# Kernel optimization log

Measured on AMD Instinct MI355X. Metric: run time of the kernel, lower is better.

## Reference

```python
import math
import jax, jax.numpy as jnp
import numpy as np

B, IB, S, D = 8, 1024, 4096, 512
WINDOW = 1
SPARSITY = 2


def setup_inputs() -> dict:
    key = jax.random.key(0)
    ks = jax.random.split(key, 12)
    std = 1.0 / math.sqrt(D)
    std_b2s = 1.0 / math.sqrt(IB)
    return {
        "text_feature": jax.random.normal(ks[0], (B, S, D), jnp.float32),
        "image_feature": jax.random.normal(ks[1], (B, IB, D), jnp.float32),
        "Wq": jax.random.normal(ks[2], (D, D), jnp.float32) * std,
        "bq": jax.random.normal(ks[3], (D,), jnp.float32) * std,
        "Wk": jax.random.normal(ks[4], (D, D), jnp.float32) * std,
        "bk": jax.random.normal(ks[5], (D,), jnp.float32) * std,
        "Wv": jax.random.normal(ks[6], (D, D), jnp.float32) * std,
        "bv": jax.random.normal(ks[7], (D,), jnp.float32) * std,
        # torch Linear(in=IB, out=S): weight shape (S, IB)
        "Wb2s": jax.random.normal(ks[8], (S, IB), jnp.float32) * std_b2s,
        "bb2s": jax.random.normal(ks[9], (S,), jnp.float32) * std_b2s,
    }


def _banded_softmax_weights():
    # attention_mask[i, max(0,i-w):min(S,i+w+1)] = 1 ; since IB < S this is a
    # banded 0/1 matrix over (IB, IB), then row-softmax.
    i = jnp.arange(IB)[:, None]
    j = jnp.arange(IB)[None, :]
    mask = ((j >= i - WINDOW) & (j <= i + WINDOW)).astype(jnp.float32)
    return jax.nn.softmax(mask, axis=-1)  # (IB, IB)


def reference(text_feature, image_feature, Wq, bq, Wk, bk, Wv, bv, Wb2s, bb2s):
    d_k = text_feature.shape[-1]
    q = image_feature @ Wq.T + bq            # (B, IB, D)
    k = text_feature @ Wk.T + bk              # (B, S, D)
    v = text_feature @ Wv.T + bv              # (B, S, D)

    # batch-invariant sparse attention pattern: compute once, broadcast via einsum
    aw = _banded_softmax_weights()             # (IB, IB)
    aw = aw @ Wb2s.T + bb2s                    # (IB, S)
    num_nonzero = S // SPARSITY + 2 * WINDOW
    topk_scores, topk_idx = jax.lax.top_k(aw, num_nonzero)  # (IB, nnz)
    sparse = jnp.zeros((IB, S), aw.dtype).at[jnp.arange(IB)[:, None], topk_idx].set(topk_scores)

    out = jnp.einsum('is,bsd->bid', sparse, k)                       # (B, IB, D)
    out = jnp.einsum('bid,bjd->bij', q, out) / math.sqrt(d_k)        # (B, IB, IB)
    out = out @ Wb2s.T + bb2s                                        # (B, IB, S)
    out = jnp.einsum('bis,bsd->bid', jax.nn.softmax(out, axis=-1), v)  # (B, IB, D)
    return out
```

## Files before the change

### kernel.cpp

```cpp
#include <hip/hip_runtime.h>

#define B_  8
#define IB_ 1024
#define S_  4096
#define D_  512

typedef _Float16 f16;
typedef _Float16 f16x8 __attribute__((ext_vector_type(8)));
typedef _Float16 f16x4 __attribute__((ext_vector_type(4)));
typedef float    f32x4 __attribute__((ext_vector_type(4)));

__device__ __forceinline__ void gld_lds16(const f16* g, f16* l) {
  __builtin_amdgcn_global_load_lds(
      (const __attribute__((address_space(1))) void*)g,
      (__attribute__((address_space(3))) void*)l, 16, 0, 0);
}

__global__ __launch_bounds__(256) void gemm_bt(
    const f16* __restrict__ A, const f16* __restrict__ B,
    float* __restrict__ C32, f16* __restrict__ C16,
    int M, int N, int K, int lda, int ldb, int ksplit,
    long long sAb, long long sBb, long long sCb,
    const float* __restrict__ bias_row, const float* __restrict__ bias_col,
    float scale)
{
  __shared__ f16 ldsA[2][128 * 32];
  __shared__ f16 ldsB[2][128 * 32];
  const int tid  = threadIdx.x;
  const int lane = tid & 63;
  const int wave = tid >> 6;
  const int zb   = blockIdx.z / ksplit;
  const int ks   = blockIdx.z % ksplit;
  A += (size_t)zb * (size_t)sAb;
  B += (size_t)zb * (size_t)sBb;
  const int m0 = blockIdx.y * 128;
  const int n0 = blockIdx.x * 128;
  const int wm = wave >> 1, wn = wave & 1;

  f32x4 acc[4][4];
#pragma unroll
  for (int i = 0; i < 4; ++i)
#pragma unroll
    for (int j = 0; j < 4; ++j) acc[i][j] = (f32x4){0.f, 0.f, 0.f, 0.f};

  int aoff[4], boff[4];
  const int cl = lane >> 4;
#pragma unroll
  for (int r = 0; r < 4; ++r) {
    int rowa = wm * 64 + r * 16 + (lane & 15);
    aoff[r] = rowa * 32 + (cl ^ ((rowa >> 1) & 3)) * 8;
    int rowb = wn * 64 + r * 16 + (lane & 15);
    boff[r] = rowb * 32 + (cl ^ ((rowb >> 1) & 3)) * 8;
  }
  int srow[2], scg[2];
#pragma unroll
  for (int it = 0; it < 2; ++it) {
    int ch = wave * 64 + it * 256 + lane;
    srow[it] = ch >> 2;
    scg[it]  = (ch & 3) ^ ((srow[it] >> 1) & 3);
  }

#define STAGE(bf_, k0_)                                                        \
  do {                                                                         \
    _Pragma("unroll")                                                          \
    for (int it = 0; it < 2; ++it) {                                           \
      gld_lds16(A + (size_t)(m0 + srow[it]) * (size_t)lda +                    \
                    ((k0_) + scg[it] * 8),                                     \
                &ldsA[bf_][(wave * 64 + it * 256) * 8]);                       \
      gld_lds16(B + (size_t)(n0 + srow[it]) * (size_t)ldb +                    \
                    ((k0_) + scg[it] * 8),                                     \
                &ldsB[bf_][(wave * 64 + it * 256) * 8]);                       \
    }                                                                          \
  } while (0)

  const int Kc   = K / ksplit;
  const int kbeg = ks * Kc;
  const int nt   = Kc / 32;

  STAGE(0, kbeg);
  for (int t = 0; t < nt; ++t) {
    const int cur = t & 1;
    if (t + 1 < nt) {
      STAGE(cur ^ 1, kbeg + (t + 1) * 32);
      asm volatile("s_waitcnt vmcnt(4)" ::: "memory");
    } else {
      asm volatile("s_waitcnt vmcnt(0)" ::: "memory");
    }
    __builtin_amdgcn_s_barrier();
    __builtin_amdgcn_sched_barrier(0);
    f16x8 af[4], bf[4];
#pragma unroll
    for (int r = 0; r < 4; ++r) af[r] = *(const f16x8*)&ldsA[cur][aoff[r]];
#pragma unroll
    for (int r = 0; r < 4; ++r) bf[r] = *(const f16x8*)&ldsB[cur][boff[r]];
#pragma unroll
    for (int mr = 0; mr < 4; ++mr)
#pragma unroll
      for (int nr = 0; nr < 4; ++nr)
        acc[mr][nr] = __builtin_amdgcn_mfma_f32_16x16x32_f16(
            af[mr], bf[nr], acc[mr][nr], 0, 0, 0);
    __builtin_amdgcn_sched_barrier(0);
    __builtin_amdgcn_s_barrier();
    __builtin_amdgcn_sched_barrier(0);
  }
#undef STAGE

  const size_t cz = (ksplit > 1) ? (size_t)blockIdx.z : (size_t)zb;
  float* c32 = C32 ? C32 + cz * (size_t)sCb : nullptr;
  f16*   c16 = C16 ? C16 + cz * (size_t)sCb : nullptr;
#pragma unroll
  for (int mr = 0; mr < 4; ++mr) {
#pragma unroll
    for (int r = 0; r < 4; ++r) {
      int grow = m0 + wm * 64 + mr * 16 + (lane >> 4) * 4 + r;
      float brv = bias_row ? bias_row[grow] : 0.f;
#pragma unroll
      for (int nr = 0; nr < 4; ++nr) {
        int gcol = n0 + wn * 64 + nr * 16 + (lane & 15);
        float v = acc[mr][nr][r] * scale + brv +
                  (bias_col ? bias_col[gcol] : 0.f);
        if (c32) c32[(size_t)grow * N + gcol] = v;
        else     c16[(size_t)grow * N + gcol] = (f16)v;
      }
    }
  }
}

__global__ __launch_bounds__(256) void gemm_pt(
    const f16* __restrict__ Bt, const float* __restrict__ uarr,
    const float* __restrict__ inv2, const float* __restrict__ Acs,
    const float* __restrict__ bb2s, f16* __restrict__ parts)
{
  __shared__ f16 ldsA[64 * 32];
  __shared__ f16 ldsB[2][256 * 32];
  __shared__ float cA2[1024], cB2[1024];
  const int tid  = threadIdx.x;
  const int lane = tid & 63;
  const int wave = tid >> 6;
  int id = (int)blockIdx.x;
  id = (id & 7) * 128 + (id >> 3);
  const int zb = id >> 7;
  const int rem = id & 127;
  const int mt = rem >> 3;
  const int x  = (rem >> 2) & 1;
  const int ks = rem & 3;
  const int kbeg = ks * 1024;
  const int m0 = mt * 64, n0 = x * 256;
  const f16* B = Bt + (size_t)zb * ((size_t)D_ * S_);

  const float L2E = 1.44269504088896340736f;
  for (int i = tid; i < 1024; i += 256) {
    cA2[i] = Acs[kbeg + i] * L2E;
    cB2[i] = bb2s[kbeg + i] * L2E;
  }
  const int srowA = tid >> 2;
  const int scgA  = tid & 3;
  const int spcA  = scgA ^ ((srowA >> 1) & 3);
  const float u_  = uarr[zb * IB_ + m0 + srowA];
  const float iv_ = inv2[zb * IB_ + m0 + srowA];
  const int cl = lane >> 4;
  int aoff[4], boff[4];
#pragma unroll
  for (int r = 0; r < 4; ++r) {
    int rowa = r * 16 + (lane & 15);
    aoff[r] = rowa * 32 + (cl ^ ((rowa >> 1) & 3)) * 8;
    int rowb = wave * 64 + r * 16 + (lane & 15);
    boff[r] = rowb * 32 + (cl ^ ((rowb >> 1) & 3)) * 8;
  }
  int srow[4], scg[4];
#pragma unroll
  for (int it = 0; it < 4; ++it) {
    int ch = wave * 64 + it * 256 + lane;
    srow[it] = ch >> 2;
    scg[it]  = (ch & 3) ^ ((srow[it] >> 1) & 3);
  }
  f32x4 acc[4][4];
#pragma unroll
  for (int i = 0; i < 4; ++i)
#pragma unroll
    for (int j = 0; j < 4; ++j) acc[i][j] = (f32x4){0.f, 0.f, 0.f, 0.f};

#define STAGEB(bf_, k0_)                                                       \
  do {                                                                         \
    _Pragma("unroll")                                                          \
    for (int it = 0; it < 4; ++it) {                                           \
      gld_lds16(B + (size_t)(n0 + srow[it]) * (size_t)S_ +                     \
                    ((k0_) + scg[it] * 8),                                     \
                &ldsB[bf_][(wave * 64 + it * 256) * 8]);                       \
    }                                                                          \
  } while (0)

  __syncthreads();
  STAGEB(0, kbeg);
  for (int t = 0; t < 32; ++t) {
    const int cur = t & 1;
    if (t + 1 < 32) STAGEB(cur ^ 1, kbeg + (t + 1) * 32);
    {
      const int kl = t * 32 + scgA * 8;
      f16x8 hp;
#pragma unroll
      for (int j = 0; j < 8; ++j) {
        float e = exp2f(fmaf(u_, cA2[kl + j], cB2[kl + j])) * iv_;
        hp[j] = (f16)e;
      }
      *(f16x8*)&ldsA[srowA * 32 + spcA * 8] = hp;
    }
    asm volatile("s_waitcnt lgkmcnt(0)" ::: "memory");
    __builtin_amdgcn_sched_barrier(0);
    if (t + 1 < 32) asm volatile("s_waitcnt vmcnt(4)" ::: "memory");
    else            asm volatile("s_waitcnt vmcnt(0)" ::: "memory");
    __builtin_amdgcn_s_barrier();
    __builtin_amdgcn_sched_barrier(0);
    f16x8 af[4], bf[4];
#pragma unroll
    for (int r = 0; r < 4; ++r) af[r] = *(const f16x8*)&ldsA[aoff[r]];
#pragma unroll
    for (int r = 0; r < 4; ++r) bf[r] = *(const f16x8*)&ldsB[cur][boff[r]];
    asm volatile("s_waitcnt lgkmcnt(0)" ::: "memory");
    __builtin_amdgcn_sched_barrier(0);
#pragma unroll
    for (int mr = 0; mr < 4; ++mr)
#pragma unroll
      for (int nr = 0; nr < 4; ++nr)
        acc[mr][nr] = __builtin_amdgcn_mfma_f32_16x16x32_f16(
            af[mr], bf[nr], acc[mr][nr], 0, 0, 0);
    __builtin_amdgcn_sched_barrier(0);
    __builtin_amdgcn_s_barrier();
    __builtin_amdgcn_sched_barrier(0);
  }
#undef STAGEB

  f16* cp = parts + (size_t)(zb * 4 + ks) * (size_t)(IB_ * D_);
#pragma unroll
  for (int mr = 0; mr < 4; ++mr) {
#pragma unroll
    for (int rr = 0; rr < 4; ++rr) {
      int grow = m0 + mr * 16 + (lane >> 4) * 4 + rr;
#pragma unroll
      for (int nr = 0; nr < 4; ++nr) {
        int gcol = n0 + wave * 64 + nr * 16 + (lane & 15);
        cp[(size_t)grow * D_ + gcol] = (f16)acc[mr][nr][rr];
      }
    }
  }
}

__global__ __launch_bounds__(256) void reduce_ks4_f16(
    const f16x8* __restrict__ p, f16x8* __restrict__ o, unsigned n8)
{
  const unsigned pb8 = (IB_ * D_) / 8;
  unsigned i = blockIdx.x * 256u + threadIdx.x;
  const unsigned stride = gridDim.x * 256u;
  for (; i < n8; i += stride) {
    unsigned g = i / pb8, r = i - g * pb8;
    size_t base = ((size_t)g * 4u) * pb8 + r;
    float acc[8] = {0.f, 0.f, 0.f, 0.f, 0.f, 0.f, 0.f, 0.f};
#pragma unroll
    for (int ks = 0; ks < 4; ++ks) {
      f16x8 v = p[base + (size_t)ks * pb8];
#pragma unroll
      for (int j = 0; j < 8; ++j) acc[j] += (float)v[j];
    }
    f16x8 h;
#pragma unroll
    for (int j = 0; j < 8; ++j) h[j] = (f16)acc[j];
    o[i] = h;
  }
}

__global__ __launch_bounds__(256) void reduce_ks2_bias(
    const f16x8* __restrict__ p, const float* __restrict__ bias,
    float4* __restrict__ o, unsigned n8)
{
  unsigned i = blockIdx.x * 256u + threadIdx.x;
  const unsigned stride = gridDim.x * 256u;
  for (; i < n8; i += stride) {
    f16x8 a = p[i];
    f16x8 b = p[i + (size_t)n8];
    const int c0 = (int)((i * 8u) & (D_ - 1));
    float4 lo, hi;
    lo.x = (float)a[0] + (float)b[0] + bias[c0 + 0];
    lo.y = (float)a[1] + (float)b[1] + bias[c0 + 1];
    lo.z = (float)a[2] + (float)b[2] + bias[c0 + 2];
    lo.w = (float)a[3] + (float)b[3] + bias[c0 + 3];
    hi.x = (float)a[4] + (float)b[4] + bias[c0 + 4];
    hi.y = (float)a[5] + (float)b[5] + bias[c0 + 5];
    hi.z = (float)a[6] + (float)b[6] + bias[c0 + 6];
    hi.w = (float)a[7] + (float)b[7] + bias[c0 + 7];
    o[(size_t)i * 2]     = lo;
    o[(size_t)i * 2 + 1] = hi;
  }
}

__global__ __launch_bounds__(256) void cvt_f32_to_f16(
    const float* __restrict__ in, f16* __restrict__ out, unsigned n)
{
  unsigned i = (blockIdx.x * 256u + threadIdx.x) * 4u;
  if (i >= n) return;
  const float4 v = *(const float4*)(in + i);
  f16x4 h;
  h[0] = (f16)v.x; h[1] = (f16)v.y; h[2] = (f16)v.z; h[3] = (f16)v.w;
  *(f16x4*)(out + i) = h;
}

__global__ __launch_bounds__(256) void transpose_text(
    const float* __restrict__ in, f16* __restrict__ out)
{
  __shared__ float t[32][65];
  const int b = blockIdx.z;
  const int s0 = blockIdx.x * 64, d0 = blockIdx.y * 32;
  const int dx = threadIdx.x & 31;
  const int sy = threadIdx.x >> 5;
  const float* ip = in + ((size_t)b * S_ + s0) * D_ + d0;
#pragma unroll
  for (int j = 0; j < 8; ++j) {
    int sl = j * 8 + sy;
    t[dx][sl] = ip[(size_t)sl * D_ + dx];
  }
  __syncthreads();
  const int sx = threadIdx.x & 63;
  const int dy = threadIdx.x >> 6;
  f16* op = out + ((size_t)b * D_ + d0) * S_ + s0;
#pragma unroll
  for (int j = 0; j < 8; ++j) {
    int dl = j * 4 + dy;
    op[(size_t)dl * S_ + sx] = (f16)t[dl][sx];
  }
}

__global__ __launch_bounds__(256) void rowsum_kernel(
    const float* __restrict__ W, float* __restrict__ out)
{
  int s = blockIdx.x;
  const float* row = W + (size_t)s * IB_;
  float acc = 0.f;
  for (int j = threadIdx.x; j < IB_; j += 256) acc += row[j];
  __shared__ float red[4];
#pragma unroll
  for (int o = 32; o >= 1; o >>= 1) acc += __shfl_xor(acc, o);
  if ((threadIdx.x & 63) == 0) red[threadIdx.x >> 6] = acc;
  __syncthreads();
  if (threadIdx.x == 0) out[s] = red[0] + red[1] + red[2] + red[3];
}

__device__ __forceinline__ unsigned fkey(float x) {
  unsigned u = __float_as_uint(x);
  return (u & 0x80000000u) ? ~u : (u | 0x80000000u);
}

__global__ __launch_bounds__(256) void prep_mu(
    const float* __restrict__ Acs, const float* __restrict__ bb2s,
    float* __restrict__ muk, float* __restrict__ rhat)
{
  __shared__ float vals[S_];
  __shared__ unsigned hist[256];
  __shared__ unsigned sprefix;
  __shared__ int srem;
  __shared__ float rred[4];
  const float e1 = 2.71828182845904523536f;
  const float Z = 3.f * e1 + (float)(IB_ - 3);
  const float alpha = 1.f / Z;
  for (int s = threadIdx.x; s < S_; s += 256)
    vals[s] = alpha * Acs[s] + bb2s[s];
  if (threadIdx.x == 0) { sprefix = 0u; srem = S_ / 2 + 2; }
  __syncthreads();
  for (int shift = 24; shift >= 0; shift -= 8) {
    hist[threadIdx.x] = 0u;
    __syncthreads();
    unsigned pfx = sprefix;
    unsigned himask = (shift == 24) ? 0u : (0xFFFFFFFFu << (shift + 8));
    for (int s = threadIdx.x; s < S_; s += 256) {
      unsigned key = fkey(vals[s]);
      if ((key & himask) == (pfx & himask))
        atomicAdd(&hist[(key >> shift) & 255u], 1u);
    }
    __syncthreads();
    if (threadIdx.x == 0) {
      int rem = srem;
      unsigned acc = 0;
      int b = 255;
      for (; b > 0; --b) {
        unsigned c = hist[b];
        if (acc + c >= (unsigned)rem) break;
        acc += c;
      }
      sprefix = pfx | ((unsigned)b << shift);
      srem = rem - (int)acc;
    }
    __syncthreads();
  }
  const unsigned T = sprefix;
  float myrs = 0.f;
  for (int s = threadIdx.x; s < S_; s += 256) {
    float v = vals[s];
    bool keep = fkey(v) >= T;
    muk[s] = keep ? v : 0.f;
    if (keep) myrs += v;
  }
#pragma unroll
  for (int o = 32; o >= 1; o >>= 1) myrs += __shfl_xor(myrs, o);
  if ((threadIdx.x & 63) == 0) rred[threadIdx.x >> 6] = myrs;
  __syncthreads();
  if (threadIdx.x == 0) rhat[0] = rred[0] + rred[1] + rred[2] + rred[3];
}

__global__ __launch_bounds__(256) void that_partial(
    const float* __restrict__ text, const float* __restrict__ muk,
    float* __restrict__ tp)
{
  const int d = blockIdx.x * 256 + threadIdx.x;
  const int c = blockIdx.y;
  const int b = blockIdx.z;
  const float* tb = text + ((size_t)b * S_ + (size_t)c * 128) * D_ + d;
  float acc = 0.f;
  for (int s = 0; s < 128; ++s) {
    float m = muk[c * 128 + s];
    if (m != 0.f) acc += m * tb[(size_t)s * D_];
  }
  tp[((size_t)b * 32 + c) * D_ + d] = acc;
}

__global__ __launch_bounds__(256) void tt_reduce(
    const float* __restrict__ tp, float* __restrict__ tt)
{
  const int d = blockIdx.x * 256 + threadIdx.x;
  const int b = blockIdx.y;
  float acc = 0.f;
#pragma unroll
  for (int c = 0; c < 32; ++c) acc += tp[((size_t)b * 32 + c) * D_ + d];
  tt[(size_t)b * D_ + d] = acc;
}

__global__ __launch_bounds__(256) void mhat2_kernel(
    const float* __restrict__ tt, const float* __restrict__ Wk,
    const float* __restrict__ bk, const float* __restrict__ rhat,
    float* __restrict__ mh)
{
  __shared__ float tl[B_ * D_];
  const int t = threadIdx.x;
  for (int i = t; i < B_ * D_; i += 256) tl[i] = tt[i];
  __syncthreads();
  const int r = blockIdx.x;
  const int lane = t & 63, wave = t >> 6;
  const float* wr = Wk + (size_t)r * D_;
  float w[8];
#pragma unroll
  for (int j = 0; j < 8; ++j) w[j] = wr[lane + 64 * j];
  const float bkr = bk[r] * rhat[0];
#pragma unroll
  for (int bb = 0; bb < 2; ++bb) {
    const int b = wave * 2 + bb;
    float acc = 0.f;
#pragma unroll
    for (int j = 0; j < 8; ++j) acc += w[j] * tl[b * D_ + lane + 64 * j];
#pragma unroll
    for (int o = 32; o >= 1; o >>= 1) acc += __shfl_xor(acc, o);
    if (lane == 0) mh[b * D_ + r] = acc + bkr;
  }
}

__global__ __launch_bounds__(256) void ypart_kernel(
    const float* __restrict__ Wq, const float* __restrict__ mh,
    float* __restrict__ yp)
{
  __shared__ float ms[B_ * 64];
  const int t = threadIdx.x;
  const int d = blockIdx.x * 256 + t;
  const int c = blockIdx.y;
  for (int i = t; i < B_ * 64; i += 256) {
    int b = i >> 6, rr = i & 63;
    ms[i] = mh[b * D_ + c * 64 + rr];
  }
  __syncthreads();
  float acc[8] = {0.f, 0.f, 0.f, 0.f, 0.f, 0.f, 0.f, 0.f};
  for (int rr = 0; rr < 64; ++rr) {
    float wv = Wq[(size_t)(c * 64 + rr) * D_ + d];
#pragma unroll
    for (int b = 0; b < 8; ++b) acc[b] += wv * ms[b * 64 + rr];
  }
#pragma unroll
  for (int b = 0; b < 8; ++b)
    yp[((size_t)c * 8 + b) * D_ + d] = acc[b];
}

__global__ __launch_bounds__(256) void yred_kernel(
    const float* __restrict__ yp, float* __restrict__ y)
{
  const int d = blockIdx.x * 256 + threadIdx.x;
  const int b = blockIdx.y;
  float acc = 0.f;
#pragma unroll
  for (int c = 0; c < 8; ++c) acc += yp[((size_t)c * 8 + b) * D_ + d];
  y[(size_t)b * D_ + d] = acc;
}

__global__ __launch_bounds__(256) void cb_kernel(
    const float* __restrict__ bq, const float* __restrict__ mh,
    float* __restrict__ cb)
{
  const int lane = threadIdx.x & 63, wave = threadIdx.x >> 6;
#pragma unroll
  for (int bb = 0; bb < 2; ++bb) {
    const int b = wave * 2 + bb;
    float acc = 0.f;
#pragma unroll
    for (int j = 0; j < 8; ++j) {
      int k = lane + 64 * j;
      acc += bq[k] * mh[b * D_ + k];
    }
#pragma unroll
    for (int o = 32; o >= 1; o >>= 1) acc += __shfl_xor(acc, o);
    if (lane == 0) cb[b] = acc;
  }
}

__global__ __launch_bounds__(256) void u_kernel(
    const float* __restrict__ img, const float* __restrict__ y,
    const float* __restrict__ cb, float scl, float* __restrict__ u)
{
  const int lane = threadIdx.x & 63, wave = threadIdx.x >> 6;
  const int row = blockIdx.x * 4 + wave;
  const int b = row >> 10;
  const float* ir = img + (size_t)row * D_;
  const float* yb = y + (size_t)b * D_;
  float acc = 0.f;
#pragma unroll
  for (int j = 0; j < 8; ++j) {
    int d = lane + 64 * j;
    acc += ir[d] * yb[d];
  }
#pragma unroll
  for (int o = 32; o >= 1; o >>= 1) acc += __shfl_xor(acc, o);
  if (lane == 0) u[row] = (acc + cb[b]) * scl;
}

__global__ __launch_bounds__(256) void pstat_kernel(
    const float* __restrict__ uarr, const float* __restrict__ Acs,
    const float* __restrict__ bb2s, float* __restrict__ inv2)
{
  const int row = blockIdx.x;
  const int t = threadIdx.x;
  __shared__ float red[4];
  const float u = uarr[row];
  float v[16];
  float mx = -3.4e38f;
#pragma unroll
  for (int j = 0; j < 16; ++j) {
    int s = t + 256 * j;
    v[j] = fmaf(u, Acs[s], bb2s[s]);
    mx = fmaxf(mx, v[j]);
  }
#pragma unroll
  for (int o = 32; o >= 1; o >>= 1) mx = fmaxf(mx, __shfl_xor(mx, o));
  if ((t & 63) == 0) red[t >> 6] = mx;
  __syncthreads();
  mx = fmaxf(fmaxf(red[0], red[1]), fmaxf(red[2], red[3]));
  __syncthreads();
  float sum = 0.f;
#pragma unroll
  for (int j = 0; j < 16; ++j) sum += __expf(v[j] - mx);
#pragma unroll
  for (int o = 32; o >= 1; o >>= 1) sum += __shfl_xor(sum, o);
  if ((t & 63) == 0) red[t >> 6] = sum;
  __syncthreads();
  if (t == 0) {
    float Zs = red[0] + red[1] + red[2] + red[3];
    inv2[row] = __expf(-mx) / Zs;
  }
}

extern "C" void kernel_launch(void* const* d_in, const int* in_sizes, int n_in,
                              void* d_out, int out_size, void* d_ws, size_t ws_size,
                              hipStream_t stream)
{
  const float* text = (const float*)d_in[0];
  const float* img  = (const float*)d_in[1];
  const float* Wq   = (const float*)d_in[2];
  const float* bq   = (const float*)d_in[3];
  const float* Wk   = (const float*)d_in[4];
  const float* bk   = (const float*)d_in[5];
  const float* Wv   = (const float*)d_in[6];
  const float* bv   = (const float*)d_in[7];
  const float* Wb2s = (const float*)d_in[8];
  const float* bb2s = (const float*)d_in[9];
  float* outp = (float*)d_out;
  char* ws = (char*)d_ws;

  const long long ID = (long long)IB_ * D_;
  const size_t MB = 1048576ull;

  const size_t NEED = 96 * MB;
  if (ws_size < NEED) return;

  f16*   textT   = (f16*)(ws + 0);
  f16*   pt16    = (f16*)(ws + 32 * MB);
  f16*   partsPT = (f16*)(ws + 40 * MB);
  f16*   partsO  = (f16*)(ws + 72 * MB);
  f16*   wv16    = (f16*)(ws + 88 * MB);
  const size_t SB = 89 * MB;
  float* Acs  = (float*)(ws + SB);
  float* muk  = (float*)(ws + SB + 16384);
  float* tp   = (float*)(ws + SB + 32768);
  float* tt   = (float*)(ws + SB + 557056);
  float* mh   = (float*)(ws + SB + 573440);
  float* rhat = (float*)(ws + SB + 589824);
  float* yp   = (float*)(ws + SB + 593920);
  float* y    = (float*)(ws + SB + 724992);
  float* cb   = (float*)(ws + SB + 741376);
  float* u    = (float*)(ws + SB + 745472);
  float* inv2 = (float*)(ws + SB + 778240);

  dim3 blk(256);
  const float scl = 0.04419417382415922f;

  rowsum_kernel<<<S_, blk, 0, stream>>>(Wb2s, Acs);
  prep_mu<<<1, blk, 0, stream>>>(Acs, bb2s, muk, rhat);
  that_partial<<<dim3(2, 32, B_), blk, 0, stream>>>(text, muk, tp);
  tt_reduce<<<dim3(2, B_), blk, 0, stream>>>(tp, tt);
  mhat2_kernel<<<512, blk, 0, stream>>>(tt, Wk, bk, rhat, mh);
  ypart_kernel<<<dim3(2, 8), blk, 0, stream>>>(Wq, mh, yp);
  yred_kernel<<<dim3(2, B_), blk, 0, stream>>>(yp, y);
  cb_kernel<<<1, blk, 0, stream>>>(bq, mh, cb);
  u_kernel<<<(B_ * IB_) / 4, blk, 0, stream>>>(img, y, cb, scl, u);
  pstat_kernel<<<B_ * IB_, blk, 0, stream>>>(u, Acs, bb2s, inv2);
  transpose_text<<<dim3(S_/64, D_/32, B_), blk, 0, stream>>>(text, textT);
  gemm_pt<<<1024, blk, 0, stream>>>(textT, u, inv2, Acs, bb2s, partsPT);
  reduce_ks4_f16<<<1024, blk, 0, stream>>>(
      (const f16x8*)partsPT, (f16x8*)pt16, (unsigned)((B_ * ID) / 8));
  cvt_f32_to_f16<<<(D_*D_)/1024, blk, 0, stream>>>(Wv, wv16, D_*D_);
  gemm_bt<<<dim3(D_/128, (B_*IB_)/128, 2), blk, 0, stream>>>(
      pt16, wv16, nullptr, partsO, B_*IB_, D_, D_, D_, D_, 2,
      0, 0, (long long)B_ * ID, nullptr, nullptr, 1.f);
  reduce_ks2_bias<<<1024, blk, 0, stream>>>(
      (const f16x8*)partsO, bv, (float4*)outp, (unsigned)((B_ * ID) / 8));
}
```

Before: 217.2 us.

## Widen gemm_pt tile to full D and fuse u and pstat kernels

gemm_pt now covers the full 512-wide N per block instead of two 256-wide halves. This halves the grid and avoids computing the exp-based A tile twice per row block, at the cost of twice the accumulators and LDS per block. The u_kernel and pstat_kernel are merged into one launch that computes u per row and then its softmax stats, which removes a launch and a round trip of u through memory. The larger register and LDS footprint may lower occupancy.

```diff
diff --git a/kernel.cpp b/kernel.cpp
--- a/kernel.cpp
+++ b/kernel.cpp
@@ -132,20 +132,19 @@
     const float* __restrict__ bb2s, f16* __restrict__ parts)
 {
   __shared__ f16 ldsA[64 * 32];
-  __shared__ f16 ldsB[2][256 * 32];
+  __shared__ f16 ldsB[2][512 * 32];
   __shared__ float cA2[1024], cB2[1024];
   const int tid  = threadIdx.x;
   const int lane = tid & 63;
   const int wave = tid >> 6;
   int id = (int)blockIdx.x;
-  id = (id & 7) * 128 + (id >> 3);
-  const int zb = id >> 7;
-  const int rem = id & 127;
-  const int mt = rem >> 3;
-  const int x  = (rem >> 2) & 1;
-  const int ks = rem & 3;
+  id = (id & 7) * 64 + (id >> 3);
+  const int zb  = id >> 6;
+  const int rem = id & 63;
+  const int mt  = rem >> 2;
+  const int ks  = rem & 3;
   const int kbeg = ks * 1024;
-  const int m0 = mt * 64, n0 = x * 256;
+  const int m0 = mt * 64;
   const f16* B = Bt + (size_t)zb * ((size_t)D_ * S_);
 
   const float L2E = 1.44269504088896340736f;
@@ -159,34 +158,36 @@
   const float u_  = uarr[zb * IB_ + m0 + srowA];
   const float iv_ = inv2[zb * IB_ + m0 + srowA];
   const int cl = lane >> 4;
-  int aoff[4], boff[4];
+  int aoff[4], boff[8];
 #pragma unroll
   for (int r = 0; r < 4; ++r) {
     int rowa = r * 16 + (lane & 15);
     aoff[r] = rowa * 32 + (cl ^ ((rowa >> 1) & 3)) * 8;
-    int rowb = wave * 64 + r * 16 + (lane & 15);
+  }
+#pragma unroll
+  for (int r = 0; r < 8; ++r) {
+    int rowb = wave * 128 + r * 16 + (lane & 15);
     boff[r] = rowb * 32 + (cl ^ ((rowb >> 1) & 3)) * 8;
   }
-  int srow[4], scg[4];
-#pragma unroll
-  for (int it = 0; it < 4; ++it) {
-    int ch = wave * 64 + it * 256 + lane;
+  int srow[8], scg[8];
+#pragma unroll
+  for (int it = 0; it < 8; ++it) {
+    int ch = it * 256 + tid;
     srow[it] = ch >> 2;
     scg[it]  = (ch & 3) ^ ((srow[it] >> 1) & 3);
   }
-  f32x4 acc[4][4];
+  f32x4 acc[4][8];
 #pragma unroll
   for (int i = 0; i < 4; ++i)
 #pragma unroll
-    for (int j = 0; j < 4; ++j) acc[i][j] = (f32x4){0.f, 0.f, 0.f, 0.f};
+    for (int j = 0; j < 8; ++j) acc[i][j] = (f32x4){0.f, 0.f, 0.f, 0.f};
 
 #define STAGEB(bf_, k0_)                                                       \
   do {                                                                         \
     _Pragma("unroll")                                                          \
-    for (int it = 0; it < 4; ++it) {                                           \
-      gld_lds16(B + (size_t)(n0 + srow[it]) * (size_t)S_ +                     \
-                    ((k0_) + scg[it] * 8),                                     \
-                &ldsB[bf_][(wave * 64 + it * 256) * 8]);                       \
+    for (int it = 0; it < 8; ++it) {                                           \
+      gld_lds16(B + (size_t)srow[it] * (size_t)S_ + ((k0_) + scg[it] * 8),     \
+                &ldsB[bf_][(it * 256 + tid) * 8]);                             \
     }                                                                          \
   } while (0)
 
@@ -207,21 +208,21 @@
     }
     asm volatile("s_waitcnt lgkmcnt(0)" ::: "memory");
     __builtin_amdgcn_sched_barrier(0);
-    if (t + 1 < 32) asm volatile("s_waitcnt vmcnt(4)" ::: "memory");
+    if (t + 1 < 32) asm volatile("s_waitcnt vmcnt(8)" ::: "memory");
     else            asm volatile("s_waitcnt vmcnt(0)" ::: "memory");
     __builtin_amdgcn_s_barrier();
     __builtin_amdgcn_sched_barrier(0);
-    f16x8 af[4], bf[4];
+    f16x8 af[4], bf[8];
 #pragma unroll
     for (int r = 0; r < 4; ++r) af[r] = *(const f16x8*)&ldsA[aoff[r]];
 #pragma unroll
-    for (int r = 0; r < 4; ++r) bf[r] = *(const f16x8*)&ldsB[cur][boff[r]];
+    for (int r = 0; r < 8; ++r) bf[r] = *(const f16x8*)&ldsB[cur][boff[r]];
     asm volatile("s_waitcnt lgkmcnt(0)" ::: "memory");
     __builtin_amdgcn_sched_barrier(0);
 #pragma unroll
     for (int mr = 0; mr < 4; ++mr)
 #pragma unroll
-      for (int nr = 0; nr < 4; ++nr)
+      for (int nr = 0; nr < 8; ++nr)
         acc[mr][nr] = __builtin_amdgcn_mfma_f32_16x16x32_f16(
             af[mr], bf[nr], acc[mr][nr], 0, 0, 0);
     __builtin_amdgcn_sched_barrier(0);
@@ -237,8 +238,8 @@
     for (int rr = 0; rr < 4; ++rr) {
       int grow = m0 + mr * 16 + (lane >> 4) * 4 + rr;
 #pragma unroll
-      for (int nr = 0; nr < 4; ++nr) {
-        int gcol = n0 + wave * 64 + nr * 16 + (lane & 15);
+      for (int nr = 0; nr < 8; ++nr) {
+        int gcol = wave * 128 + nr * 16 + (lane & 15);
         cp[(size_t)grow * D_ + gcol] = (f16)acc[mr][nr][rr];
       }
     }
@@ -514,34 +515,31 @@
   }
 }
 
-__global__ __launch_bounds__(256) void u_kernel(
+__global__ __launch_bounds__(256) void upstat_kernel(
     const float* __restrict__ img, const float* __restrict__ y,
-    const float* __restrict__ cb, float scl, float* __restrict__ u)
-{
-  const int lane = threadIdx.x & 63, wave = threadIdx.x >> 6;
-  const int row = blockIdx.x * 4 + wave;
+    const float* __restrict__ cbv, const float* __restrict__ Acs,
+    const float* __restrict__ bb2s, float scl,
+    float* __restrict__ uo, float* __restrict__ inv2)
+{
+  const int row = blockIdx.x;
   const int b = row >> 10;
+  const int t = threadIdx.x;
+  __shared__ float red[4];
+  __shared__ float ubc;
   const float* ir = img + (size_t)row * D_;
   const float* yb = y + (size_t)b * D_;
-  float acc = 0.f;
-#pragma unroll
-  for (int j = 0; j < 8; ++j) {
-    int d = lane + 64 * j;
-    acc += ir[d] * yb[d];
-  }
-#pragma unroll
-  for (int o = 32; o >= 1; o >>= 1) acc += __shfl_xor(acc, o);
-  if (lane == 0) u[row] = (acc + cb[b]) * scl;
-}
-
-__global__ __launch_bounds__(256) void pstat_kernel(
-    const float* __restrict__ uarr, const float* __restrict__ Acs,
-    const float* __restrict__ bb2s, float* __restrict__ inv2)
-{
-  const int row = blockIdx.x;
-  const int t = threadIdx.x;
-  __shared__ float red[4];
-  const float u = uarr[row];
+  float du = ir[t] * yb[t] + ir[t + 256] * yb[t + 256];
+#pragma unroll
+  for (int o = 32; o >= 1; o >>= 1) du += __shfl_xor(du, o);
+  if ((t & 63) == 0) red[t >> 6] = du;
+  __syncthreads();
+  if (t == 0) {
+    float uu = (red[0] + red[1] + red[2] + red[3] + cbv[b]) * scl;
+    ubc = uu;
+    uo[row] = uu;
+  }
+  __syncthreads();
+  const float u = ubc;
   float v[16];
   float mx = -3.4e38f;
 #pragma unroll
@@ -621,10 +619,10 @@
   ypart_kernel<<<dim3(2, 8), blk, 0, stream>>>(Wq, mh, yp);
   yred_kernel<<<dim3(2, B_), blk, 0, stream>>>(yp, y);
   cb_kernel<<<1, blk, 0, stream>>>(bq, mh, cb);
-  u_kernel<<<(B_ * IB_) / 4, blk, 0, stream>>>(img, y, cb, scl, u);
-  pstat_kernel<<<B_ * IB_, blk, 0, stream>>>(u, Acs, bb2s, inv2);
+  upstat_kernel<<<B_ * IB_, blk, 0, stream>>>(img, y, cb, Acs, bb2s, scl,
+                                              u, inv2);
   transpose_text<<<dim3(S_/64, D_/32, B_), blk, 0, stream>>>(text, textT);
-  gemm_pt<<<1024, blk, 0, stream>>>(textT, u, inv2, Acs, bb2s, partsPT);
+  gemm_pt<<<512, blk, 0, stream>>>(textT, u, inv2, Acs, bb2s, partsPT);
   reduce_ks4_f16<<<1024, blk, 0, stream>>>(
       (const f16x8*)partsPT, (f16x8*)pt16, (unsigned)((B_ * ID) / 8));
   cvt_f32_to_f16<<<(D_*D_)/1024, blk, 0, stream>>>(Wv, wv16, D_*D_);
```

After: 247.7 us. 14.0% more time.
